# Performance work log

Measured on AMD Instinct MI355X. Metric: run time of the kernel, lower is better.

Reference implementation:

```python
import jax, jax.numpy as jnp
import numpy as np

N_USERS = 100000
N_ITEMS = 50000
N_NODES = N_USERS + N_ITEMS
NNZ = 4800000
EMB = 64
N_LAYERS = 3
BATCH = 4096
REG = 1e-5


def setup_inputs() -> dict:
    key = jax.random.key(0)
    ks = jax.random.split(key, 12)
    rows = jax.random.randint(ks[0], (NNZ,), 0, N_NODES, dtype=jnp.int32)
    cols = jax.random.randint(ks[1], (NNZ,), 0, N_NODES, dtype=jnp.int32)
    # normalized-Laplacian-like positive edge weights
    vals = jax.random.uniform(ks[2], (NNZ,), dtype=jnp.float32) * 0.05
    user_emb = jax.random.normal(ks[3], (N_USERS, EMB), dtype=jnp.float32) * 0.1
    item_emb = jax.random.normal(ks[4], (N_ITEMS, EMB), dtype=jnp.float32) * 0.1
    # xavier-ish scale for 64x64: std ~= 0.125
    W_one = jax.random.normal(ks[5], (N_LAYERS, EMB, EMB), dtype=jnp.float32) * 0.125
    b_one = jax.random.normal(ks[6], (N_LAYERS, EMB), dtype=jnp.float32) * 0.125
    W_two = jax.random.normal(ks[7], (N_LAYERS, EMB, EMB), dtype=jnp.float32) * 0.125
    b_two = jax.random.normal(ks[8], (N_LAYERS, EMB), dtype=jnp.float32) * 0.125
    u = jax.random.randint(ks[9], (BATCH,), 0, N_USERS, dtype=jnp.int32)
    i = jax.random.randint(ks[10], (BATCH,), 0, N_ITEMS, dtype=jnp.int32)
    j = jax.random.randint(ks[11], (BATCH,), 0, N_ITEMS, dtype=jnp.int32)
    return {"rows": rows, "cols": cols, "vals": vals, "user_emb": user_emb,
            "item_emb": item_emb, "W_one": W_one, "b_one": b_one,
            "W_two": W_two, "b_two": b_two, "u": u, "i": i, "j": j}


def _spmm(rows, cols, vals, x):
    # sparse.mm(L, x): gather rows of x at cols, scale by edge vals, scatter-add into rows
    return jax.ops.segment_sum(vals[:, None] * x[cols], rows, num_segments=N_NODES)


def reference(rows, cols, vals, user_emb, item_emb, W_one, b_one, W_two, b_two, u, i, j):
    ego = jnp.concatenate([user_emb, item_emb], axis=0)  # [N_NODES, EMB]
    finals = [ego]
    for k in range(N_LAYERS):
        xk = finals[k]
        side_L = _spmm(rows, cols, vals, xk)          # L @ x
        side_LI = side_L + xk                          # (L + I) @ x
        simple = side_LI @ W_one[k] + b_one[k]
        interaction = (side_L * xk) @ W_two[k] + b_two[k]
        ego_k = jax.nn.leaky_relu(simple + interaction)  # mess_dropout=0 -> identity
        norm = ego_k / jnp.maximum(jnp.linalg.norm(ego_k, axis=1, keepdims=True), 1e-12)
        finals.append(norm)
    final = jnp.concatenate(finals, axis=1)            # [N_NODES, EMB*(1+N_LAYERS)]
    u_emb = final[u]
    p_emb = final[N_USERS + i]
    n_emb = final[N_USERS + j]
    y_ui = jnp.sum(u_emb * p_emb, axis=1)
    y_uj = jnp.sum(u_emb * n_emb, axis=1)
    bpr_loss = -jnp.mean(jax.nn.log_sigmoid(y_ui - y_uj))
    l2norm = (jnp.sum(u_emb ** 2) / 2.0 + jnp.sum(p_emb ** 2) / 2.0 + jnp.sum(n_emb ** 2) / 2.0) / BATCH
    return bpr_loss + REG * l2norm
```

## Files before the change

### kernel.cpp

```cpp
#include <hip/hip_runtime.h>
#include <hip/hip_bf16.h>
#include <math.h>

#define N_USERS 100000
#define N_ITEMS 50000
#define N_NODES 150000
#define NNZ     4800000
#define EMB     64
#define BATCH   4096
#define REG_C   1e-5f

#define ROWB    512
#define NBK     293
#define PADC    17408
#define CSTRIDE 16
#define P1_EPB  8192
#define NB_P1   ((NNZ + P1_EPB - 1) / P1_EPB)
#define NB_PACK 2344
#define NB_ACC0 1024

#define LROW    36

typedef short short8 __attribute__((ext_vector_type(8)));
typedef float f32x4  __attribute__((ext_vector_type(4)));
typedef float f32x2  __attribute__((ext_vector_type(2)));

static __device__ __forceinline__ unsigned short f2bf(float f) {
    unsigned u = __float_as_uint(f);
    u = u + 0x7FFFu + ((u >> 16) & 1u);
    return (unsigned short)(u >> 16);
}
static __device__ __forceinline__ unsigned pk2(float lo, float hi) {
    return (unsigned)f2bf(lo) | ((unsigned)f2bf(hi) << 16);
}
static __device__ __forceinline__ float blo(unsigned a) { return __uint_as_float(a << 16); }
static __device__ __forceinline__ float bhi(unsigned a) { return __uint_as_float(a & 0xFFFF0000u); }

static __device__ __forceinline__ unsigned pkq4(float f0, float f1, float f2, float f3) {
    int v = __builtin_amdgcn_cvt_pk_fp8_f32(f0, f1, 0, false);
    v = __builtin_amdgcn_cvt_pk_fp8_f32(f2, f3, v, true);
    return (unsigned)v;
}

static __device__ __forceinline__ void eload(const int2* p_, int& c, float& v) {
    unsigned long long w = __builtin_nontemporal_load((const unsigned long long*)p_);
    c = (int)(unsigned)(w & 0xFFFFFFFFu);
    v = __int_as_float((int)(unsigned)(w >> 32));
}
static __device__ __forceinline__ int ntl(const int* p_) {
    return __builtin_nontemporal_load(p_);
}
static __device__ __forceinline__ float ntlf(const float* p_) {
    return __builtin_nontemporal_load(p_);
}

__global__ __launch_bounds__(256) void p1_bin_kernel(
    const int* __restrict__ rows, const int* __restrict__ cols,
    const float* __restrict__ vals, int* __restrict__ gcursor,
    int2* __restrict__ binned,
    const float* __restrict__ ue, const float* __restrict__ ie,
    unsigned int* __restrict__ xh, unsigned int* __restrict__ xq,
    const int* __restrict__ u, const int* __restrict__ ii,
    const int* __restrict__ jj,
    float* __restrict__ dui, float* __restrict__ duj, float* __restrict__ l2a) {
    __shared__ int rowbuf[P1_EPB];
    __shared__ int hist[NBK];
    __shared__ int base[NBK];
    int t = threadIdx.x;
    int bid = blockIdx.x;

    if (bid >= NB_P1 + NB_PACK) {
        int b = (bid - NB_P1 - NB_PACK) * 4 + (t >> 6);
        int lane = t & 63;
        float uv = ue[(size_t)u[b] * 64 + lane];
        float pv = ie[(size_t)ii[b] * 64 + lane];
        float nv = ie[(size_t)jj[b] * 64 + lane];
        float a = uv * pv, c = uv * nv, l = uv * uv + pv * pv + nv * nv;
        #pragma unroll
        for (int o = 32; o > 0; o >>= 1) {
            a += __shfl_xor(a, o, 64);
            c += __shfl_xor(c, o, 64);
            l += __shfl_xor(l, o, 64);
        }
        if (lane == 0) { dui[b] = a; duj[b] = c; l2a[b] = l; }
        return;
    }
    if (bid >= NB_P1) {
        int g0 = ((bid - NB_P1) * 256 + t) * 2;
        #pragma unroll
        for (int g = g0; g < g0 + 2; ++g) {
            if (g >= N_NODES * 8) break;
            const float4* src;
            if (g < N_USERS * 8) src = (const float4*)ue + (size_t)g * 2;
            else src = (const float4*)ie + (size_t)(g - N_USERS * 8) * 2;
            float4 a = src[0], b = src[1];
            uint4 h;
            h.x = pk2(a.x, a.y); h.y = pk2(a.z, a.w);
            h.z = pk2(b.x, b.y); h.w = pk2(b.z, b.w);
            ((uint4*)xh)[g] = h;
            uint2 q;
            q.x = pkq4(a.x, a.y, a.z, a.w);
            q.y = pkq4(b.x, b.y, b.z, b.w);
            ((uint2*)xq)[g] = q;
        }
        return;
    }

    int e0 = bid * P1_EPB;
    int nE = NNZ - e0; if (nE > P1_EPB) nE = P1_EPB;
    for (int i = t; i < nE; i += 256) rowbuf[i] = ntl(&rows[e0 + i]);
    for (int b = t; b < NBK; b += 256) hist[b] = 0;
    __syncthreads();
    for (int i = t; i < nE; i += 256) atomicAdd(&hist[rowbuf[i] >> 9], 1);
    __syncthreads();
    for (int b = t; b < NBK; b += 256) {
        int h = hist[b];
        base[b] = (h > 0) ? atomicAdd(&gcursor[b * CSTRIDE], h) : 0;
        hist[b] = 0;
    }
    __syncthreads();
    for (int i = t; i < nE; i += 256) {
        int r = rowbuf[i];
        int b = r >> 9;
        int rk = atomicAdd(&hist[b], 1);
        int rel = base[b] + rk;
        if (rel < PADC)
            binned[(size_t)b * PADC + rel] =
                make_int2(ntl(&cols[e0 + i]) | ((r & 511) << 18),
                          __float_as_int(ntlf(&vals[e0 + i])));
    }
}

__global__ __launch_bounds__(256) void p2_sort_kernel(
    const int* __restrict__ gcursor, const int2* __restrict__ binned,
    int2* __restrict__ csr, int* __restrict__ start, int* __restrict__ cnt) {
    __shared__ int hist[ROWB];
    __shared__ int excl[ROWB];
    int b = blockIdx.x;
    int t = threadIdx.x;
    size_t bbase = (size_t)b * PADC;
    int n = gcursor[b * CSTRIDE];
    if (n > PADC) n = PADC;
    hist[t] = 0; hist[t + 256] = 0;
    __syncthreads();
    for (int i = t; i < n; i += 256)
        atomicAdd(&hist[(binned[bbase + i].x >> 18) & 511], 1);
    __syncthreads();
    excl[t] = hist[t]; excl[t + 256] = hist[t + 256];
    __syncthreads();
    for (int o = 1; o < ROWB; o <<= 1) {
        int i1 = t + 256;
        int v0 = (t >= o) ? excl[t - o] : 0;
        int v1 = (i1 >= o) ? excl[i1 - o] : 0;
        __syncthreads();
        excl[t] += v0; excl[i1] += v1;
        __syncthreads();
    }
    int rowsInB = N_NODES - b * ROWB;
    if (rowsInB > ROWB) rowsInB = ROWB;
    for (int rr = t; rr < ROWB; rr += 256) {
        int s = excl[rr] - hist[rr];
        if (rr < rowsInB) {
            start[b * ROWB + rr] = (int)bbase + s;
            cnt[b * ROWB + rr]   = hist[rr];
        }
        excl[rr] = s;
    }
    __syncthreads();
    for (int i = t; i < n; i += 256) {
        int2 rec = binned[bbase + i];
        int rl = (rec.x >> 18) & 511;
        int p = atomicAdd(&excl[rl], 1);
        csr[bbase + p] = make_int2(rec.x & 0x3FFFF, rec.y);
    }
}

__global__ __launch_bounds__(256) void spmm_csr_kernel(
    const int* __restrict__ start, const int* __restrict__ cnt,
    const int2* __restrict__ edges, const unsigned int* __restrict__ xq,
    float* __restrict__ out) {
    int row = blockIdx.x * 4 + (threadIdx.x >> 6);
    if (row >= N_NODES) return;
    int lane = threadIdx.x & 63;
    int eg = lane >> 4;
    int p  = lane & 15;
    int s = start[row];
    int n = cnt[row];
    float a0 = 0.f, a1 = 0.f, a2 = 0.f, a3 = 0.f;
    int k = 0;
    for (; k + 32 <= n; k += 32) {
        int c[8]; float v[8];
        #pragma unroll
        for (int j = 0; j < 8; ++j) eload(&edges[s + k + 4 * j + eg], c[j], v[j]);
        #pragma unroll
        for (int j = 0; j < 8; ++j) {
            unsigned q = xq[(size_t)c[j] * 16 + p];
            f32x2 lo = __builtin_amdgcn_cvt_pk_f32_fp8(q, false);
            f32x2 hi = __builtin_amdgcn_cvt_pk_f32_fp8(q, true);
            a0 = fmaf(v[j], lo[0], a0);
            a1 = fmaf(v[j], lo[1], a1);
            a2 = fmaf(v[j], hi[0], a2);
            a3 = fmaf(v[j], hi[1], a3);
        }
    }
    while (k < n) {
        #pragma unroll
        for (int j = 0; j < 4; ++j) {
            int off = k + 4 * j + eg;
            bool valid = off < n;
            int c; float v;
            eload(&edges[s + (valid ? off : 0)], c, v);
            if (!valid) v = 0.f;
            unsigned q = xq[(size_t)c * 16 + p];
            f32x2 lo = __builtin_amdgcn_cvt_pk_f32_fp8(q, false);
            f32x2 hi = __builtin_amdgcn_cvt_pk_f32_fp8(q, true);
            a0 = fmaf(v, lo[0], a0);
            a1 = fmaf(v, lo[1], a1);
            a2 = fmaf(v, hi[0], a2);
            a3 = fmaf(v, hi[1], a3);
        }
        k += 16;
    }
    a0 += __shfl_xor(a0, 16, 64); a0 += __shfl_xor(a0, 32, 64);
    a1 += __shfl_xor(a1, 16, 64); a1 += __shfl_xor(a1, 32, 64);
    a2 += __shfl_xor(a2, 16, 64); a2 += __shfl_xor(a2, 32, 64);
    a3 += __shfl_xor(a3, 16, 64); a3 += __shfl_xor(a3, 32, 64);
    if (eg == 0)
        ((float4*)out)[(size_t)row * 16 + p] = make_float4(a0, a1, a2, a3);
}

__global__ __launch_bounds__(256) void dense_kernel(
    unsigned int* xh, unsigned int* xq, const float* __restrict__ sideL,
    const float* __restrict__ W1, const float* __restrict__ b1,
    const float* __restrict__ W2, const float* __restrict__ b2)
{
    __shared__ unsigned asl[64 * LROW];
    __shared__ unsigned apr[64 * LROW];
    __shared__ unsigned wt1[64 * LROW];
    __shared__ unsigned wt2[64 * LROW];

    int t = threadIdx.x;
    int r0 = blockIdx.x * 64;

    #pragma unroll
    for (int i = 0; i < 4; ++i) {
        int idx = i * 256 + t;
        int kk = idx >> 4;
        int ng = idx & 15;
        float4 w1v = ((const float4*)W1)[idx];
        float4 w2v = ((const float4*)W2)[idx];
        unsigned short* s1 = (unsigned short*)wt1;
        unsigned short* s2 = (unsigned short*)wt2;
        int c0 = 4 * ng;
        s1[(c0 + 0) * (2 * LROW) + kk] = f2bf(w1v.x);
        s1[(c0 + 1) * (2 * LROW) + kk] = f2bf(w1v.y);
        s1[(c0 + 2) * (2 * LROW) + kk] = f2bf(w1v.z);
        s1[(c0 + 3) * (2 * LROW) + kk] = f2bf(w1v.w);
        s2[(c0 + 0) * (2 * LROW) + kk] = f2bf(w2v.x);
        s2[(c0 + 1) * (2 * LROW) + kk] = f2bf(w2v.y);
        s2[(c0 + 2) * (2 * LROW) + kk] = f2bf(w2v.z);
        s2[(c0 + 3) * (2 * LROW) + kk] = f2bf(w2v.w);
    }

    #pragma unroll
    for (int i = 0; i < 2; ++i) {
        int q = i * 256 + t;
        int row = q >> 3;
        int u4 = q & 7;
        uint4 h = make_uint4(0, 0, 0, 0);
        float4 s0 = make_float4(0.f, 0.f, 0.f, 0.f);
        float4 s1 = make_float4(0.f, 0.f, 0.f, 0.f);
        if (r0 + row < N_NODES) {
            h  = ((const uint4*)xh)[(size_t)(r0 + row) * 8 + u4];
            s0 = ((const float4*)sideL)[(size_t)(r0 + row) * 16 + 2 * u4];
            s1 = ((const float4*)sideL)[(size_t)(r0 + row) * 16 + 2 * u4 + 1];
        }
        float x0 = blo(h.x), x1 = bhi(h.x), x2 = blo(h.y), x3 = bhi(h.y);
        float x4 = blo(h.z), x5 = bhi(h.z), x6 = blo(h.w), x7 = bhi(h.w);
        uint4 sa, pa;
        sa.x = pk2(x0 + s0.x, x1 + s0.y); sa.y = pk2(x2 + s0.z, x3 + s0.w);
        sa.z = pk2(x4 + s1.x, x5 + s1.y); sa.w = pk2(x6 + s1.z, x7 + s1.w);
        pa.x = pk2(x0 * s0.x, x1 * s0.y); pa.y = pk2(x2 * s0.z, x3 * s0.w);
        pa.z = pk2(x4 * s1.x, x5 * s1.y); pa.w = pk2(x6 * s1.z, x7 * s1.w);
        *(uint4*)&asl[row * LROW + 4 * u4] = sa;
        *(uint4*)&apr[row * LROW + 4 * u4] = pa;
    }
    __syncthreads();

    int l = t & 63, wv = t >> 6;
    int q4 = l >> 4, mr = l & 15;
    int abase = (wv * 16 + mr) * LROW + 4 * q4;
    short8 aS0 = *(const short8*)&asl[abase];
    short8 aS1 = *(const short8*)&asl[abase + 16];
    short8 aP0 = *(const short8*)&apr[abase];
    short8 aP1 = *(const short8*)&apr[abase + 16];

    float lr[4][4];
    float rowss[4] = {0.f, 0.f, 0.f, 0.f};
    #pragma unroll
    for (int nb = 0; nb < 4; ++nb) {
        int wbase = (nb * 16 + mr) * LROW + 4 * q4;
        short8 b10 = *(const short8*)&wt1[wbase];
        short8 b11 = *(const short8*)&wt1[wbase + 16];
        short8 b20 = *(const short8*)&wt2[wbase];
        short8 b21 = *(const short8*)&wt2[wbase + 16];
        f32x4 acc = {0.f, 0.f, 0.f, 0.f};
        acc = __builtin_amdgcn_mfma_f32_16x16x32_bf16(aS0, b10, acc, 0, 0, 0);
        acc = __builtin_amdgcn_mfma_f32_16x16x32_bf16(aS1, b11, acc, 0, 0, 0);
        acc = __builtin_amdgcn_mfma_f32_16x16x32_bf16(aP0, b20, acc, 0, 0, 0);
        acc = __builtin_amdgcn_mfma_f32_16x16x32_bf16(aP1, b21, acc, 0, 0, 0);
        float bias = b1[nb * 16 + mr] + b2[nb * 16 + mr];
        #pragma unroll
        for (int r = 0; r < 4; ++r) {
            float v = acc[r] + bias;
            float lrv = v > 0.f ? v : 0.01f * v;
            lr[nb][r] = lrv;
            rowss[r] += lrv * lrv;
        }
    }
    #pragma unroll
    for (int o = 1; o < 16; o <<= 1) {
        #pragma unroll
        for (int r = 0; r < 4; ++r) rowss[r] += __shfl_xor(rowss[r], o, 64);
    }
    float inv[4];
    #pragma unroll
    for (int r = 0; r < 4; ++r) inv[r] = 1.f / fmaxf(sqrtf(rowss[r]), 1e-12f);

    __syncthreads();
    unsigned short* os = (unsigned short*)wt1;
    #pragma unroll
    for (int nb = 0; nb < 4; ++nb) {
        #pragma unroll
        for (int r = 0; r < 4; ++r) {
            int rloc = wv * 16 + q4 * 4 + r;
            os[rloc * (2 * LROW) + nb * 16 + mr] = f2bf(lr[nb][r] * inv[r]);
        }
    }
    __syncthreads();

    #pragma unroll
    for (int i = 0; i < 2; ++i) {
        int q = i * 256 + t;
        int row = q >> 3, u4 = q & 7;
        if (r0 + row < N_NODES) {
            uint4 h = *(const uint4*)&wt1[row * LROW + 4 * u4];
            ((uint4*)xh)[(size_t)(r0 + row) * 8 + u4] = h;
            uint2 qq;
            qq.x = pkq4(blo(h.x), bhi(h.x), blo(h.y), bhi(h.y));
            qq.y = pkq4(blo(h.z), bhi(h.z), blo(h.w), bhi(h.w));
            ((uint2*)xq)[(size_t)(r0 + row) * 8 + u4] = qq;
        }
    }
}

__global__ void accB_kernel(const unsigned int* __restrict__ xh,
                            const int* __restrict__ u, const int* __restrict__ ii,
                            const int* __restrict__ jj,
                            float* __restrict__ dui, float* __restrict__ duj,
                            float* __restrict__ l2a) {
    int t = threadIdx.x;
    int lane = t & 63;
    int half = lane >> 5, p = lane & 31;
    int b = blockIdx.x * 8 + (t >> 6) * 2 + half;
    unsigned ua = xh[(size_t)u[b] * 32 + p];
    unsigned pa = xh[(size_t)(N_USERS + ii[b]) * 32 + p];
    unsigned na = xh[(size_t)(N_USERS + jj[b]) * 32 + p];
    float u0 = blo(ua), u1 = bhi(ua);
    float p0 = blo(pa), p1 = bhi(pa);
    float n0 = blo(na), n1 = bhi(na);
    float a = u0 * p0 + u1 * p1;
    float c = u0 * n0 + u1 * n1;
    float l = u0 * u0 + u1 * u1 + p0 * p0 + p1 * p1 + n0 * n0 + n1 * n1;
    #pragma unroll
    for (int o = 16; o > 0; o >>= 1) {
        a += __shfl_xor(a, o, 64);
        c += __shfl_xor(c, o, 64);
        l += __shfl_xor(l, o, 64);
    }
    if (p == 0) { dui[b] += a; duj[b] += c; l2a[b] += l; }
}

__global__ void final_kernel(const float* __restrict__ dui, const float* __restrict__ duj,
                             const float* __restrict__ l2a, float* __restrict__ out) {
    __shared__ float sh[4];
    int t = threadIdx.x;
    float s = 0.f;
    for (int b = t; b < BATCH; b += 256) {
        float diff = dui[b] - duj[b];
        float ls = (diff >= 0.f) ? -log1pf(expf(-diff)) : (diff - log1pf(expf(diff)));
        s += -ls + REG_C * 0.5f * l2a[b];
    }
    #pragma unroll
    for (int o = 32; o > 0; o >>= 1) s += __shfl_xor(s, o, 64);
    int wave = t >> 6, lane = t & 63;
    if (lane == 0) sh[wave] = s;
    __syncthreads();
    if (t == 0) out[0] = (sh[0] + sh[1] + sh[2] + sh[3]) / (float)BATCH;
}

extern "C" void kernel_launch(void* const* d_in, const int* in_sizes, int n_in,
                              void* d_out, int out_size, void* d_ws, size_t ws_size,
                              hipStream_t stream) {
    const int*   rows     = (const int*)d_in[0];
    const int*   cols     = (const int*)d_in[1];
    const float* vals     = (const float*)d_in[2];
    const float* user_emb = (const float*)d_in[3];
    const float* item_emb = (const float*)d_in[4];
    const float* W_one    = (const float*)d_in[5];
    const float* b_one    = (const float*)d_in[6];
    const float* W_two    = (const float*)d_in[7];
    const float* b_two    = (const float*)d_in[8];
    const int*   u        = (const int*)d_in[9];
    const int*   ii       = (const int*)d_in[10];
    const int*   jj       = (const int*)d_in[11];

    unsigned int* Xh  = (unsigned int*)d_ws;
    unsigned int* Xq  = Xh + (size_t)N_NODES * 32;
    int2* binned      = (int2*)(Xq + (size_t)N_NODES * 16);
    float* B          = (float*)binned;
    int2* csr         = binned + (size_t)NBK * PADC;
    int*  gcursor     = (int*)(csr + (size_t)NBK * PADC);
    int*  startA      = gcursor + NBK * CSTRIDE;
    int*  cntA        = startA + 150016;
    float* dui        = (float*)(cntA + 150016);
    float* duj        = dui + BATCH;
    float* l2a        = duj + BATCH;

    (void)hipMemsetAsync(gcursor, 0, NBK * CSTRIDE * sizeof(int), stream);

    p1_bin_kernel<<<NB_P1 + NB_PACK + NB_ACC0, 256, 0, stream>>>(
        rows, cols, vals, gcursor, binned,
        user_emb, item_emb, Xh, Xq, u, ii, jj, dui, duj, l2a);
    p2_sort_kernel<<<NBK, 256, 0, stream>>>(gcursor, binned, csr, startA, cntA);

    for (int k = 0; k < 3; ++k) {
        spmm_csr_kernel<<<(N_NODES + 3) / 4, 256, 0, stream>>>(startA, cntA, csr, Xq, B);
        dense_kernel<<<(N_NODES + 63) / 64, 256, 0, stream>>>(
            Xh, Xq, B, W_one + k * 4096, b_one + k * 64,
            W_two + k * 4096, b_two + k * 64);
        accB_kernel<<<BATCH / 8, 256, 0, stream>>>(Xh, u, ii, jj, dui, duj, l2a);
    }

    final_kernel<<<1, 256, 0, stream>>>(dui, duj, l2a, (float*)d_out);
}
```

Measured before the change: 645.8 us.

## Stage binned edges in LDS for coalesced writes; store SpMM output as bf16

The binning pass now scans the per-block bucket histogram, scatters edge records into a shared-memory staging buffer grouped by bucket, then writes them out contiguously per bucket. A binary search over the bucket offsets locates each record's bucket. This is meant to turn scattered global writes into runs of coalesced ones, at the cost of more LDS, extra barriers and a halved edges-per-block count. Separately, the SpMM output is stored as packed bf16 instead of fp32, which halves the intermediate traffic into the dense kernel but adds rounding error.

New measurement: 634.6 us. Within noise of the previous version (-1.7%).

```diff
diff --git a/kernel.cpp b/kernel.cpp
--- a/kernel.cpp
+++ b/kernel.cpp
@@ -14,7 +14,7 @@
 #define NBK     293
 #define PADC    17408
 #define CSTRIDE 16
-#define P1_EPB  8192
+#define P1_EPB  4096
 #define NB_P1   ((NNZ + P1_EPB - 1) / P1_EPB)
 #define NB_PACK 2344
 #define NB_ACC0 1024
@@ -63,9 +63,11 @@
     const int* __restrict__ u, const int* __restrict__ ii,
     const int* __restrict__ jj,
     float* __restrict__ dui, float* __restrict__ duj, float* __restrict__ l2a) {
-    __shared__ int rowbuf[P1_EPB];
+    __shared__ int2 staged[P1_EPB];
     __shared__ int hist[NBK];
-    __shared__ int base[NBK];
+    __shared__ int lofs[NBK];
+    __shared__ int baseg[NBK];
+    __shared__ int scanx[512];
     int t = threadIdx.x;
     int bid = blockIdx.x;
 
@@ -108,26 +110,50 @@
 
     int e0 = bid * P1_EPB;
     int nE = NNZ - e0; if (nE > P1_EPB) nE = P1_EPB;
-    for (int i = t; i < nE; i += 256) rowbuf[i] = ntl(&rows[e0 + i]);
+
     for (int b = t; b < NBK; b += 256) hist[b] = 0;
     __syncthreads();
-    for (int i = t; i < nE; i += 256) atomicAdd(&hist[rowbuf[i] >> 9], 1);
-    __syncthreads();
+    for (int i = t; i < nE; i += 256) atomicAdd(&hist[rows[e0 + i] >> 9], 1);
+    __syncthreads();
+
+    scanx[t]       = (t < NBK) ? hist[t] : 0;
+    scanx[t + 256] = (t + 256 < NBK) ? hist[t + 256] : 0;
+    __syncthreads();
+    for (int o = 1; o < 512; o <<= 1) {
+        int i1 = t + 256;
+        int v0 = (t >= o) ? scanx[t - o] : 0;
+        int v1 = (i1 >= o) ? scanx[i1 - o] : 0;
+        __syncthreads();
+        scanx[t] += v0; scanx[i1] += v1;
+        __syncthreads();
+    }
     for (int b = t; b < NBK; b += 256) {
         int h = hist[b];
-        base[b] = (h > 0) ? atomicAdd(&gcursor[b * CSTRIDE], h) : 0;
-        hist[b] = 0;
-    }
-    __syncthreads();
+        lofs[b]  = scanx[b] - h;
+        baseg[b] = (h > 0) ? atomicAdd(&gcursor[b * CSTRIDE], h) : 0;
+        hist[b]  = 0;
+    }
+    __syncthreads();
+
     for (int i = t; i < nE; i += 256) {
-        int r = rowbuf[i];
+        int r = rows[e0 + i];
         int b = r >> 9;
-        int rk = atomicAdd(&hist[b], 1);
-        int rel = base[b] + rk;
+        int slot = lofs[b] + atomicAdd(&hist[b], 1);
+        staged[slot] = make_int2(ntl(&cols[e0 + i]) | ((r & 511) << 18),
+                                 __float_as_int(ntlf(&vals[e0 + i])));
+    }
+    __syncthreads();
+
+    for (int s = t; s < nE; s += 256) {
+        int2 rec = staged[s];
+        int lo = 0, hi = NBK - 1;
+        while (lo < hi) {
+            int mid = (lo + hi + 1) >> 1;
+            if (lofs[mid] <= s) lo = mid; else hi = mid - 1;
+        }
+        int rel = baseg[lo] + (s - lofs[lo]);
         if (rel < PADC)
-            binned[(size_t)b * PADC + rel] =
-                make_int2(ntl(&cols[e0 + i]) | ((r & 511) << 18),
-                          __float_as_int(ntlf(&vals[e0 + i])));
+            binned[(size_t)lo * PADC + rel] = rec;
     }
 }
 
@@ -178,7 +204,7 @@
 __global__ __launch_bounds__(256) void spmm_csr_kernel(
     const int* __restrict__ start, const int* __restrict__ cnt,
     const int2* __restrict__ edges, const unsigned int* __restrict__ xq,
-    float* __restrict__ out) {
+    unsigned int* __restrict__ out) {
     int row = blockIdx.x * 4 + (threadIdx.x >> 6);
     if (row >= N_NODES) return;
     int lane = threadIdx.x & 63;
@@ -225,12 +251,16 @@
     a1 += __shfl_xor(a1, 16, 64); a1 += __shfl_xor(a1, 32, 64);
     a2 += __shfl_xor(a2, 16, 64); a2 += __shfl_xor(a2, 32, 64);
     a3 += __shfl_xor(a3, 16, 64); a3 += __shfl_xor(a3, 32, 64);
-    if (eg == 0)
-        ((float4*)out)[(size_t)row * 16 + p] = make_float4(a0, a1, a2, a3);
+    if (eg == 0) {
+        uint2 o2;
+        o2.x = pk2(a0, a1);
+        o2.y = pk2(a2, a3);
+        ((uint2*)out)[(size_t)row * 16 + p] = o2;
+    }
 }
 
 __global__ __launch_bounds__(256) void dense_kernel(
-    unsigned int* xh, unsigned int* xq, const float* __restrict__ sideL,
+    unsigned int* xh, unsigned int* xq, const unsigned int* __restrict__ sideL,
     const float* __restrict__ W1, const float* __restrict__ b1,
     const float* __restrict__ W2, const float* __restrict__ b2)
 {
@@ -267,21 +297,21 @@
         int q = i * 256 + t;
         int row = q >> 3;
         int u4 = q & 7;
-        uint4 h = make_uint4(0, 0, 0, 0);
-        float4 s0 = make_float4(0.f, 0.f, 0.f, 0.f);
-        float4 s1 = make_float4(0.f, 0.f, 0.f, 0.f);
+        uint4 h  = make_uint4(0, 0, 0, 0);
+        uint4 sb = make_uint4(0, 0, 0, 0);
         if (r0 + row < N_NODES) {
             h  = ((const uint4*)xh)[(size_t)(r0 + row) * 8 + u4];
-            s0 = ((const float4*)sideL)[(size_t)(r0 + row) * 16 + 2 * u4];
-            s1 = ((const float4*)sideL)[(size_t)(r0 + row) * 16 + 2 * u4 + 1];
+            sb = ((const uint4*)sideL)[(size_t)(r0 + row) * 8 + u4];
         }
         float x0 = blo(h.x), x1 = bhi(h.x), x2 = blo(h.y), x3 = bhi(h.y);
         float x4 = blo(h.z), x5 = bhi(h.z), x6 = blo(h.w), x7 = bhi(h.w);
+        float d0 = blo(sb.x), d1 = bhi(sb.x), d2 = blo(sb.y), d3 = bhi(sb.y);
+        float d4 = blo(sb.z), d5 = bhi(sb.z), d6 = blo(sb.w), d7 = bhi(sb.w);
         uint4 sa, pa;
-        sa.x = pk2(x0 + s0.x, x1 + s0.y); sa.y = pk2(x2 + s0.z, x3 + s0.w);
-        sa.z = pk2(x4 + s1.x, x5 + s1.y); sa.w = pk2(x6 + s1.z, x7 + s1.w);
-        pa.x = pk2(x0 * s0.x, x1 * s0.y); pa.y = pk2(x2 * s0.z, x3 * s0.w);
-        pa.z = pk2(x4 * s1.x, x5 * s1.y); pa.w = pk2(x6 * s1.z, x7 * s1.w);
+        sa.x = pk2(x0 + d0, x1 + d1); sa.y = pk2(x2 + d2, x3 + d3);
+        sa.z = pk2(x4 + d4, x5 + d5); sa.w = pk2(x6 + d6, x7 + d7);
+        pa.x = pk2(x0 * d0, x1 * d1); pa.y = pk2(x2 * d2, x3 * d3);
+        pa.z = pk2(x4 * d4, x5 * d5); pa.w = pk2(x6 * d6, x7 * d7);
         *(uint4*)&asl[row * LROW + 4 * u4] = sa;
         *(uint4*)&apr[row * LROW + 4 * u4] = pa;
     }
@@ -418,7 +448,7 @@
     unsigned int* Xh  = (unsigned int*)d_ws;
     unsigned int* Xq  = Xh + (size_t)N_NODES * 32;
     int2* binned      = (int2*)(Xq + (size_t)N_NODES * 16);
-    float* B          = (float*)binned;
+    unsigned int* B   = (unsigned int*)binned;
     int2* csr         = binned + (size_t)NBK * PADC;
     int*  gcursor     = (int*)(csr + (size_t)NBK * PADC);
     int*  startA      = gcursor + NBK * CSTRIDE;
```
